# Kernel optimization log

Measured on AMD Instinct MI355X. Metric: run time of the kernel, lower is better.

The kernel has to match this reference:

```python
import jax, jax.numpy as jnp
import numpy as np

# Scatter2Operator config (matches init_kwargs)
NUM_HEADS = 16   # dims[2] / glob_size
GLOB_SIZE = 64
HEAD_SIZE = 64   # dims[2] / num_heads


def setup_inputs() -> dict:
    key = jax.random.key(0)
    ks = jax.random.split(key, 6)
    B, N, G, D0, D2 = 8, 4096, 64, 1024, 1024
    scale = 0.02
    return {
        "x0": jax.random.normal(ks[0], (B, G, D0), jnp.float32),
        "x2": jax.random.normal(ks[1], (B, N, D2), jnp.float32),
        "Wk": jax.random.normal(ks[2], (NUM_HEADS * GLOB_SIZE, D2), jnp.float32) * scale,
        "Wp": jax.random.normal(ks[3], (NUM_HEADS * HEAD_SIZE, D0), jnp.float32) * scale,
        "Wo": jax.random.normal(ks[4], (D2, NUM_HEADS * HEAD_SIZE), jnp.float32) * scale,
        "bo": jnp.zeros((D2,), jnp.float32),
    }


def reference(x0, x2, Wk, Wp, Wo, bo):
    # x2: [B, N, D2] -> kernel scores; x0: [B, G, D0] -> premise values.
    B, N, _ = x2.shape
    H, G, Dh = NUM_HEADS, GLOB_SIZE, HEAD_SIZE
    # kernel = softmax over glob slots (dropout is identity in eval mode)
    k = jnp.einsum('bnd,kd->bnk', x2, Wk).reshape(B, N, H, G)
    k = jax.nn.softmax(k, axis=-1)                      # [B, N, H, G]
    # premise projection: [B, G, H, Dh]
    p = jnp.einsum('bgd,kd->bgk', x0, Wp).reshape(B, G, H, Dh)
    # attention-like gather over the G global slots, per head
    pred = jnp.einsum('bnhg,bghd->bnhd', k, p)          # [B, N, H, Dh]
    pred = pred.reshape(B, N, H * Dh)
    # writer linear (with bias)
    return jnp.einsum('bnk,dk->bnd', pred, Wo) + bo
```

## Files before the change

### kernel.cpp

```cpp
#include <hip/hip_runtime.h>


using bf16x8 = __attribute__((ext_vector_type(8))) __bf16;
using f32x4  = __attribute__((ext_vector_type(4))) float;

__device__ __forceinline__ unsigned short f2b(float f) {
  unsigned u = __float_as_uint(f);
  u += 0x7fffu + ((u >> 16) & 1u);
  return (unsigned short)(u >> 16);
}

__global__ void cvt_all(const float* __restrict__ x2, unsigned short* __restrict__ x2b, int n0,
                        const float* __restrict__ x0, unsigned short* __restrict__ x0b, int n1,
                        const float* __restrict__ Wk, unsigned short* __restrict__ Wkb, int n2,
                        const float* __restrict__ Wp, unsigned short* __restrict__ Wpb, int n3,
                        const float* __restrict__ Wo, unsigned short* __restrict__ Wob, int n4)
{
  const int ntot = n0 + n1 + n2 + n3 + n4;
  int i = blockIdx.x * blockDim.x + threadIdx.x;
  const int stride = gridDim.x * blockDim.x;
  for (; i < ntot; i += stride) {
    const float* src; unsigned short* dst; int j = i;
    if (j < n0) { src = x2; dst = x2b; }
    else if ((j -= n0) < n1) { src = x0; dst = x0b; }
    else if ((j -= n1) < n2) { src = Wk; dst = Wkb; }
    else if ((j -= n2) < n3) { src = Wp; dst = Wpb; }
    else { j -= n3; src = Wo; dst = Wob; }
    float4 v = reinterpret_cast<const float4*>(src)[j];
    ushort4 o;
    o.x = f2b(v.x); o.y = f2b(v.y); o.z = f2b(v.z); o.w = f2b(v.w);
    reinterpret_cast<ushort4*>(dst)[j] = o;
  }
}

#define GLOAD_LDS(gsrc, ldst) __builtin_amdgcn_global_load_lds(                 \
    (const __attribute__((address_space(1))) unsigned int*)(gsrc),              \
    (__attribute__((address_space(3))) unsigned int*)(ldst), 16, 0, 0)

__device__ __forceinline__ void glds16(const unsigned short* g, unsigned ldsoff) {
  asm volatile("s_mov_b32 m0, %0\n\t"
               "global_load_lds_dwordx4 %1, off"
               :: "s"(ldsoff), "v"(g) : "memory");
}

#define BARRIER() __builtin_amdgcn_s_barrier()
#define VMC4()   asm volatile("s_waitcnt vmcnt(4)" ::: "memory")
#define VMC0()   asm volatile("s_waitcnt vmcnt(0)" ::: "memory")

__launch_bounds__(256)
__global__ void qtp(const unsigned short* __restrict__ x0b,
                    const unsigned short* __restrict__ Wpb,
                    const unsigned short* __restrict__ Wob,
                    unsigned short* __restrict__ Qtb)
{
  __shared__ __align__(16) unsigned short Pl[64 * 72];
  __shared__ __align__(16) unsigned short work[16384];

  const int bx = blockIdx.x;
  const int z  = blockIdx.z;
  const int b  = z >> 4, h = z & 15;

  const int tid  = threadIdx.x;
  const int lane = tid & 63;
  const int wid  = tid >> 6;
  const int lr   = lane & 15;
  const int hi   = lane >> 4;

  const int wr1 = (wid >> 1) * 32, wc1 = (wid & 1) * 32;
  f32x4 acc1[2][2] = {};

  int srow[2], skc[2];
#pragma unroll
  for (int j = 0; j < 2; ++j) {
    int i = j * 256 + tid;
    srow[j] = i >> 3;
    skc[j]  = ((i & 7) ^ (srow[j] & 7)) * 8;
  }
  const unsigned short* aSrc = x0b + (long)b * 65536;
  const unsigned short* bSrc = Wpb + (long)h * 64 * 1024;

  for (int kt = 0; kt < 1024; kt += 64) {
    __syncthreads();
#pragma unroll
    for (int j = 0; j < 2; ++j) {
      int i = j * 256 + tid;
      GLOAD_LDS(aSrc + (long)srow[j] * 1024 + kt + skc[j], &work[i * 8]);
      GLOAD_LDS(bSrc + (long)srow[j] * 1024 + kt + skc[j], &work[4096 + i * 8]);
    }
    __syncthreads();

    bf16x8 af[2][2], bf[2][2];
#pragma unroll
    for (int m = 0; m < 2; ++m) {
      const int rowA = wr1 + m * 16 + lr;
      const int rowB = wc1 + m * 16 + lr;
#pragma unroll
      for (int ks = 0; ks < 2; ++ks) {
        const int slotA = ((ks * 4 + hi) ^ (rowA & 7)) * 8;
        const int slotB = ((ks * 4 + hi) ^ (rowB & 7)) * 8;
        af[m][ks] = *(const bf16x8*)&work[rowA * 64 + slotA];
        bf[m][ks] = *(const bf16x8*)&work[4096 + rowB * 64 + slotB];
      }
    }
#pragma unroll
    for (int ks = 0; ks < 2; ++ks)
#pragma unroll
      for (int m = 0; m < 2; ++m)
#pragma unroll
        for (int n = 0; n < 2; ++n)
          acc1[m][n] = __builtin_amdgcn_mfma_f32_16x16x32_bf16(
              af[m][ks], bf[n][ks], acc1[m][n], 0, 0, 0);
  }

#pragma unroll
  for (int m = 0; m < 2; ++m)
#pragma unroll
    for (int r = 0; r < 4; ++r) {
      const int row = wr1 + m * 16 + hi * 4 + r;
#pragma unroll
      for (int n = 0; n < 2; ++n)
        Pl[row * 72 + wc1 + n * 16 + lr] = f2b(acc1[m][n][r]);
    }
  __syncthreads();

  const unsigned short* wSrc = Wob + (long)bx * 256 * 1024 + h * 64;
#pragma unroll
  for (int j = 0; j < 8; ++j) {
    int i = j * 256 + tid;
    int row = i >> 3;
    int kc  = ((i & 7) ^ (row & 7)) * 8;
    GLOAD_LDS(wSrc + (long)row * 1024 + kc, &work[i * 8]);
  }
  __syncthreads();

  const int wr2 = wid * 64;
  f32x4 acc2[4][4] = {};
  bf16x8 af2[4][2], bf2[4][2];
#pragma unroll
  for (int m = 0; m < 4; ++m) {
    const int rowA = wr2 + m * 16 + lr;
#pragma unroll
    for (int ks = 0; ks < 2; ++ks) {
      const int slotA = ((ks * 4 + hi) ^ (rowA & 7)) * 8;
      af2[m][ks] = *(const bf16x8*)&work[rowA * 64 + slotA];
    }
  }
#pragma unroll
  for (int n = 0; n < 4; ++n) {
    const int rowB = n * 16 + lr;
#pragma unroll
    for (int ks = 0; ks < 2; ++ks)
      bf2[n][ks] = *(const bf16x8*)&Pl[rowB * 72 + ks * 32 + hi * 8];
  }
#pragma unroll
  for (int ks = 0; ks < 2; ++ks)
#pragma unroll
    for (int m = 0; m < 4; ++m)
#pragma unroll
      for (int n = 0; n < 4; ++n)
        acc2[m][n] = __builtin_amdgcn_mfma_f32_16x16x32_bf16(
            af2[m][ks], bf2[n][ks], acc2[m][n], 0, 0, 0);

  unsigned short* Cq = Qtb + (long)b * 1048576 + h * 64;
#pragma unroll
  for (int n = 0; n < 4; ++n) {
    const int col = n * 16 + lr;
#pragma unroll
    for (int m = 0; m < 4; ++m)
#pragma unroll
      for (int r = 0; r < 4; ++r) {
        const int row = bx * 256 + wr2 + m * 16 + hi * 4 + r;
        Cq[(long)row * 1024 + col] = f2b(acc2[m][n][r]);
      }
  }
}

template<int EPI, int BATCHED>
__launch_bounds__(512)
__global__ void gemm256(const unsigned short* __restrict__ A,
                        const unsigned short* __restrict__ B,
                        void* __restrict__ Cv,
                        const float* __restrict__ bias,
                        int K, long sA, long sB, long sC)
{
  extern __shared__ __align__(16) char smem[];

  const int tid  = threadIdx.x;
  const int lane = tid & 63, wid = tid >> 6;
  const int wm = wid >> 2, wn = wid & 3;
  const int lr = lane & 15, hi = lane >> 4;
  const int swz  = (lane & 7) << 4;
  const int prow = lane >> 3;
  const int pxor = ((lane & 7) ^ prow) * 8;

  int bx, by; long abase = 0, bbase = 0, cbase = 0;
  if (BATCHED) {
    const int bid = blockIdx.x;
    const int z = bid & 7, idx = bid >> 3;
    bx = idx & 15; by = idx >> 4;
    abase = (long)z * sA; bbase = (long)z * sB; cbase = (long)z * sC;
  } else {
    const int bid = blockIdx.x;
    const int lin = (bid & 7) * 64 + (bid >> 3);
    bx = lin >> 2; by = lin & 3;
  }
  const int brow = bx * 256, bcol = by * 256;

  const unsigned short* __restrict__ Ab = A + abase;
  const unsigned short* __restrict__ Bb = B + bbase;

  unsigned short* ldsA[2] = { (unsigned short*)(smem),
                              (unsigned short*)(smem + 65536) };
  unsigned short* ldsB[2] = { (unsigned short*)(smem + 32768),
                              (unsigned short*)(smem + 98304) };
  const unsigned ldsbase =
      __builtin_amdgcn_readfirstlane((unsigned)(unsigned long long)smem);

  const long ldaL = 1024, ldbL = 1024, ldcL = 1024;

  auto stageA = [&](int buf, int h, int kt) {
    const unsigned short* s = Ab + (long)(brow + h * 128 + wid * 8 + prow) * ldaL + kt + pxor;
    unsigned d = ldsbase + (unsigned)(buf * 65536 + h * 16384 + wid * 1024);
    glds16(s, __builtin_amdgcn_readfirstlane(d));
    glds16(s + 64 * ldaL, __builtin_amdgcn_readfirstlane(d + 8192u));
  };
  auto stageB = [&](int buf, int h, int kt) {
    const unsigned short* s = Bb + (long)(bcol + h * 128 + wid * 8 + prow) * ldbL + kt + pxor;
    unsigned d = ldsbase + (unsigned)(32768 + buf * 65536 + h * 16384 + wid * 1024);
    glds16(s, __builtin_amdgcn_readfirstlane(d));
    glds16(s + 64 * ldbL, __builtin_amdgcn_readfirstlane(d + 8192u));
  };

  bf16x8 af[4][2], bloA[2][2], bloB[2][2], bhi[2][2];

  auto ldA_ = [&](int buf, int mh) {
    const unsigned short* base = ldsA[buf];
#pragma unroll
    for (int mi = 0; mi < 4; ++mi) {
      const int row = wm * 128 + mh * 64 + mi * 16 + lr;
#pragma unroll
      for (int ks = 0; ks < 2; ++ks) {
        const int cb = (ks * 64 + hi * 16) ^ swz;
        af[mi][ks] = *(const bf16x8*)(base + row * 64 + (cb >> 1));
      }
    }
  };
  auto ldBlo = [&](int buf, bf16x8 (&dst)[2][2]) {
    const unsigned short* base = ldsB[buf];
#pragma unroll
    for (int ni = 0; ni < 2; ++ni) {
      const int row = wn * 64 + ni * 16 + lr;
#pragma unroll
      for (int ks = 0; ks < 2; ++ks) {
        const int cb = (ks * 64 + hi * 16) ^ swz;
        dst[ni][ks] = *(const bf16x8*)(base + row * 64 + (cb >> 1));
      }
    }
  };
  auto ldBhi = [&](int buf) {
    const unsigned short* base = ldsB[buf];
#pragma unroll
    for (int ni = 0; ni < 2; ++ni) {
      const int row = wn * 64 + 32 + ni * 16 + lr;
#pragma unroll
      for (int ks = 0; ks < 2; ++ks) {
        const int cb = (ks * 64 + hi * 16) ^ swz;
        bhi[ni][ks] = *(const bf16x8*)(base + row * 64 + (cb >> 1));
      }
    }
  };

  f32x4 acc[8][4] = {};
  auto mmaH = [&](bf16x8 (&b)[2][2], int mh, int nh) {
    __builtin_amdgcn_s_setprio(1);
#pragma unroll
    for (int ks = 0; ks < 2; ++ks)
#pragma unroll
      for (int mi = 0; mi < 4; ++mi)
#pragma unroll
        for (int ni = 0; ni < 2; ++ni)
          acc[mh * 4 + mi][nh * 2 + ni] = __builtin_amdgcn_mfma_f32_16x16x32_bf16(
              af[mi][ks], b[ni][ks], acc[mh * 4 + mi][nh * 2 + ni], 0, 0, 0);
    __builtin_amdgcn_s_setprio(0);
  };

  stageB(0, 0, 0); stageB(0, 1, 0); stageA(0, 0, 0); stageA(0, 1, 0);
  stageB(1, 0, 64); stageB(1, 1, 64);
  VMC4(); BARRIER();
  ldBlo(0, bloA);

  const int NI = K >> 7;
#pragma unroll 1
  for (int i = 0; i < NI; ++i) {
    const int kt1 = i * 128 + 64;
    int kt2 = i * 128 + 128; if (kt2 >= K) kt2 -= K;
    int kt3 = i * 128 + 192; if (kt3 >= K) kt3 -= K;

    ldA_(0, 0); stageA(1, 0, kt1);
    BARRIER(); mmaH(bloA, 0, 0); BARRIER();
    ldBhi(0); stageA(1, 1, kt1);
    BARRIER(); mmaH(bhi, 0, 1); BARRIER();
    ldA_(0, 1); stageB(0, 0, kt2);
    BARRIER(); mmaH(bloA, 1, 0); BARRIER();
    stageB(0, 1, kt2); VMC4(); ldBlo(1, bloB);
    BARRIER(); mmaH(bhi, 1, 1); BARRIER();
    ldA_(1, 0); stageA(0, 0, kt2);
    BARRIER(); mmaH(bloB, 0, 0); BARRIER();
    ldBhi(1); stageA(0, 1, kt2);
    BARRIER(); mmaH(bhi, 0, 1); BARRIER();
    ldA_(1, 1); stageB(1, 0, kt3);
    BARRIER(); mmaH(bloB, 1, 0); BARRIER();
    stageB(1, 1, kt3); VMC4(); ldBlo(0, bloA);
    BARRIER(); mmaH(bhi, 1, 1); BARRIER();
  }
  VMC0();

  const int rowb = brow + wm * 128 + hi * 4;
  const int colb = bcol + wn * 64 + lr;

  if (EPI == 2) {
    unsigned short* C = (unsigned short*)Cv + cbase;
#pragma unroll
    for (int m = 0; m < 8; ++m) {
#pragma unroll
      for (int r = 0; r < 4; ++r) {
        float v0 = acc[m][0][r], v1 = acc[m][1][r], v2 = acc[m][2][r], v3 = acc[m][3][r];
        float mx = fmaxf(fmaxf(v0, v1), fmaxf(v2, v3));
        mx = fmaxf(mx, __shfl_xor(mx, 1));
        mx = fmaxf(mx, __shfl_xor(mx, 2));
        mx = fmaxf(mx, __shfl_xor(mx, 4));
        mx = fmaxf(mx, __shfl_xor(mx, 8));
        float e0 = __expf(v0 - mx), e1 = __expf(v1 - mx);
        float e2 = __expf(v2 - mx), e3 = __expf(v3 - mx);
        float s = e0 + e1 + e2 + e3;
        s += __shfl_xor(s, 1);
        s += __shfl_xor(s, 2);
        s += __shfl_xor(s, 4);
        s += __shfl_xor(s, 8);
        float inv = 1.0f / s;
        unsigned short* cp = C + (long)(rowb + m * 16 + r) * ldcL + colb;
        cp[0]  = f2b(e0 * inv);
        cp[16] = f2b(e1 * inv);
        cp[32] = f2b(e2 * inv);
        cp[48] = f2b(e3 * inv);
      }
    }
  } else {
    float* C = (float*)Cv + cbase;
#pragma unroll
    for (int n = 0; n < 4; ++n) {
      const int col = colb + n * 16;
      const float bv = bias[col];
#pragma unroll
      for (int m = 0; m < 8; ++m)
#pragma unroll
        for (int r = 0; r < 4; ++r)
          C[(long)(rowb + m * 16 + r) * ldcL + col] = acc[m][n][r] + bv;
    }
  }
}

extern "C" void kernel_launch(void* const* d_in, const int* in_sizes, int n_in,
                              void* d_out, int out_size, void* d_ws, size_t ws_size,
                              hipStream_t stream) {
  (void)in_sizes; (void)n_in; (void)out_size; (void)ws_size;
  const float* x0 = (const float*)d_in[0];
  const float* x2 = (const float*)d_in[1];
  const float* Wk = (const float*)d_in[2];
  const float* Wp = (const float*)d_in[3];
  const float* Wo = (const float*)d_in[4];
  const float* bo = (const float*)d_in[5];
  float* out = (float*)d_out;

  const long Bz = 8, Nn = 4096, Gg = 64, Dd = 1024;
  const long MN = Bz * Nn;

  char* ws = (char*)d_ws;
  size_t off = 0;
  auto alloc = [&](size_t bytes) {
    size_t cur = off;
    off = (cur + bytes + 255) & ~(size_t)255;
    return (unsigned short*)(ws + cur);
  };
  unsigned short* x2b = alloc(MN * Dd * 2);
  unsigned short* kb  = alloc(MN * Dd * 2);
  unsigned short* Wkb = alloc(Dd * Dd * 2);
  unsigned short* Wpb = alloc(Dd * Dd * 2);
  unsigned short* Wob = alloc(Dd * Dd * 2);
  unsigned short* x0b = alloc(Bz * Gg * Dd * 2);
  unsigned short* Qtb = alloc(Bz * Dd * Dd * 2);

  hipFuncSetAttribute(reinterpret_cast<const void*>(gemm256<2, 0>),
                      hipFuncAttributeMaxDynamicSharedMemorySize, 131072);
  hipFuncSetAttribute(reinterpret_cast<const void*>(gemm256<1, 1>),
                      hipFuncAttributeMaxDynamicSharedMemorySize, 131072);

  cvt_all<<<dim3(4096), dim3(256), 0, stream>>>(
      x2, x2b, (int)(MN * Dd / 4),
      x0, x0b, (int)(Bz * Gg * Dd / 4),
      Wk, Wkb, (int)(Dd * Dd / 4),
      Wp, Wpb, (int)(Dd * Dd / 4),
      Wo, Wob, (int)(Dd * Dd / 4));

  gemm256<2, 0><<<dim3(512, 1, 1), dim3(512), 131072, stream>>>(
      x2b, Wkb, kb, nullptr, 1024, 0, 0, 0);

  qtp<<<dim3(4, 1, 128), dim3(256), 0, stream>>>(x0b, Wpb, Wob, Qtb);

  gemm256<1, 1><<<dim3(512, 1, 1), dim3(512), 131072, stream>>>(
      kb, Qtb, (void*)out, bo, 1024,
      (long)4096 * 1024, (long)1024 * 1024, (long)4096 * 1024);
}
```

Baseline: 218.0 us.

## Restructure GEMM main loop into per-K-tile double-buffered A fragment pipeline

```diff
diff --git a/kernel.cpp b/kernel.cpp
--- a/kernel.cpp
+++ b/kernel.cpp
@@ -44,8 +44,10 @@
 }
 
 #define BARRIER() __builtin_amdgcn_s_barrier()
+#define VMC8()   asm volatile("s_waitcnt vmcnt(8)" ::: "memory")
 #define VMC4()   asm volatile("s_waitcnt vmcnt(4)" ::: "memory")
 #define VMC0()   asm volatile("s_waitcnt vmcnt(0)" ::: "memory")
+#define LGKM0()  asm volatile("s_waitcnt lgkmcnt(0)" ::: "memory")
 
 __launch_bounds__(256)
 __global__ void qtp(const unsigned short* __restrict__ x0b,
@@ -209,10 +211,6 @@
   const unsigned short* __restrict__ Ab = A + abase;
   const unsigned short* __restrict__ Bb = B + bbase;
 
-  unsigned short* ldsA[2] = { (unsigned short*)(smem),
-                              (unsigned short*)(smem + 65536) };
-  unsigned short* ldsB[2] = { (unsigned short*)(smem + 32768),
-                              (unsigned short*)(smem + 98304) };
   const unsigned ldsbase =
       __builtin_amdgcn_readfirstlane((unsigned)(unsigned long long)smem);
 
@@ -231,34 +229,41 @@
     glds16(s + 64 * ldbL, __builtin_amdgcn_readfirstlane(d + 8192u));
   };
 
-  bf16x8 af[4][2], bloA[2][2], bloB[2][2], bhi[2][2];
-
-  auto ldA_ = [&](int buf, int mh) {
-    const unsigned short* base = ldsA[buf];
+  auto ldsAp = [&](int buf) {
+    return (const unsigned short*)(smem + buf * 65536);
+  };
+  auto ldsBp = [&](int buf) {
+    return (const unsigned short*)(smem + 32768 + buf * 65536);
+  };
+
+  bf16x8 afA[4][2], afB[4][2], blo[2][2], bhi[2][2];
+
+  auto ldAx = [&](int buf, int mh, bf16x8 (&dst)[4][2]) {
+    const unsigned short* base = ldsAp(buf);
 #pragma unroll
     for (int mi = 0; mi < 4; ++mi) {
       const int row = wm * 128 + mh * 64 + mi * 16 + lr;
 #pragma unroll
       for (int ks = 0; ks < 2; ++ks) {
         const int cb = (ks * 64 + hi * 16) ^ swz;
-        af[mi][ks] = *(const bf16x8*)(base + row * 64 + (cb >> 1));
-      }
-    }
-  };
-  auto ldBlo = [&](int buf, bf16x8 (&dst)[2][2]) {
-    const unsigned short* base = ldsB[buf];
+        dst[mi][ks] = *(const bf16x8*)(base + row * 64 + (cb >> 1));
+      }
+    }
+  };
+  auto ldBlo_ = [&](int buf) {
+    const unsigned short* base = ldsBp(buf);
 #pragma unroll
     for (int ni = 0; ni < 2; ++ni) {
       const int row = wn * 64 + ni * 16 + lr;
 #pragma unroll
       for (int ks = 0; ks < 2; ++ks) {
         const int cb = (ks * 64 + hi * 16) ^ swz;
-        dst[ni][ks] = *(const bf16x8*)(base + row * 64 + (cb >> 1));
-      }
-    }
-  };
-  auto ldBhi = [&](int buf) {
-    const unsigned short* base = ldsB[buf];
+        blo[ni][ks] = *(const bf16x8*)(base + row * 64 + (cb >> 1));
+      }
+    }
+  };
+  auto ldBhi_ = [&](int buf) {
+    const unsigned short* base = ldsBp(buf);
 #pragma unroll
     for (int ni = 0; ni < 2; ++ni) {
       const int row = wn * 64 + 32 + ni * 16 + lr;
@@ -271,7 +276,7 @@
   };
 
   f32x4 acc[8][4] = {};
-  auto mmaH = [&](bf16x8 (&b)[2][2], int mh, int nh) {
+  auto mmaH = [&](bf16x8 (&a)[4][2], bf16x8 (&b)[2][2], int mh, int nh) {
     __builtin_amdgcn_s_setprio(1);
 #pragma unroll
     for (int ks = 0; ks < 2; ++ks)
@@ -280,38 +285,30 @@
 #pragma unroll
         for (int ni = 0; ni < 2; ++ni)
           acc[mh * 4 + mi][nh * 2 + ni] = __builtin_amdgcn_mfma_f32_16x16x32_bf16(
-              af[mi][ks], b[ni][ks], acc[mh * 4 + mi][nh * 2 + ni], 0, 0, 0);
+              a[mi][ks], b[ni][ks], acc[mh * 4 + mi][nh * 2 + ni], 0, 0, 0);
     __builtin_amdgcn_s_setprio(0);
   };
 
-  stageB(0, 0, 0); stageB(0, 1, 0); stageA(0, 0, 0); stageA(0, 1, 0);
-  stageB(1, 0, 64); stageB(1, 1, 64);
-  VMC4(); BARRIER();
-  ldBlo(0, bloA);
-
-  const int NI = K >> 7;
+  stageA(0, 0, 0); stageA(0, 1, 0); stageB(0, 0, 0); stageB(0, 1, 0);
+  stageA(1, 0, 64); stageA(1, 1, 64); stageB(1, 0, 64); stageB(1, 1, 64);
+  VMC8(); BARRIER();
+  ldAx(0, 0, afA); ldBlo_(0);
+
+  const int NT = K >> 6;
 #pragma unroll 1
-  for (int i = 0; i < NI; ++i) {
-    const int kt1 = i * 128 + 64;
-    int kt2 = i * 128 + 128; if (kt2 >= K) kt2 -= K;
-    int kt3 = i * 128 + 192; if (kt3 >= K) kt3 -= K;
-
-    ldA_(0, 0); stageA(1, 0, kt1);
-    BARRIER(); mmaH(bloA, 0, 0); BARRIER();
-    ldBhi(0); stageA(1, 1, kt1);
-    BARRIER(); mmaH(bhi, 0, 1); BARRIER();
-    ldA_(0, 1); stageB(0, 0, kt2);
-    BARRIER(); mmaH(bloA, 1, 0); BARRIER();
-    stageB(0, 1, kt2); VMC4(); ldBlo(1, bloB);
-    BARRIER(); mmaH(bhi, 1, 1); BARRIER();
-    ldA_(1, 0); stageA(0, 0, kt2);
-    BARRIER(); mmaH(bloB, 0, 0); BARRIER();
-    ldBhi(1); stageA(0, 1, kt2);
-    BARRIER(); mmaH(bhi, 0, 1); BARRIER();
-    ldA_(1, 1); stageB(1, 0, kt3);
-    BARRIER(); mmaH(bloB, 1, 0); BARRIER();
-    stageB(1, 1, kt3); VMC4(); ldBlo(0, bloA);
-    BARRIER(); mmaH(bhi, 1, 1); BARRIER();
+  for (int t = 0; t < NT; ++t) {
+    const int buf = t & 1, nbuf = buf ^ 1;
+    int ktn = (t + 2) * 64; if (ktn >= K) ktn -= K;
+
+    VMC8(); ldBhi_(buf);
+    BARRIER(); mmaH(afA, blo, 0, 0); BARRIER();
+    ldAx(buf, 1, afB);
+    BARRIER(); mmaH(afA, bhi, 0, 1); LGKM0(); BARRIER();
+    stageA(buf, 0, ktn); stageA(buf, 1, ktn);
+    BARRIER(); mmaH(afB, blo, 1, 0); BARRIER();
+    VMC4(); ldAx(nbuf, 0, afA); ldBlo_(nbuf);
+    stageB(buf, 0, ktn); stageB(buf, 1, ktn);
+    BARRIER(); mmaH(afB, bhi, 1, 1); BARRIER();
   }
   VMC0();
 
@@ -390,10 +387,10 @@
   unsigned short* x0b = alloc(Bz * Gg * Dd * 2);
   unsigned short* Qtb = alloc(Bz * Dd * Dd * 2);
 
-  hipFuncSetAttribute(reinterpret_cast<const void*>(gemm256<2, 0>),
-                      hipFuncAttributeMaxDynamicSharedMemorySize, 131072);
-  hipFuncSetAttribute(reinterpret_cast<const void*>(gemm256<1, 1>),
-                      hipFuncAttributeMaxDynamicSharedMemorySize, 131072);
+  (void)hipFuncSetAttribute(reinterpret_cast<const void*>(gemm256<2, 0>),
+                            hipFuncAttributeMaxDynamicSharedMemorySize, 131072);
+  (void)hipFuncSetAttribute(reinterpret_cast<const void*>(gemm256<1, 1>),
+                            hipFuncAttributeMaxDynamicSharedMemorySize, 131072);
 
   cvt_all<<<dim3(4096), dim3(256), 0, stream>>>(
       x2, x2b, (int)(MN * Dd / 4),
```

Result: slower. 230.7 us (+5.8%).
